# Kernel optimization log

Measured on AMD Instinct MI355X. Metric: run time of the kernel, lower is better.

## Reference

```python
import jax, jax.numpy as jnp
import numpy as np

TMP = 1.0          # concrete temperature (beta)
SAMPLE_BIAS = 0.0  # self.sample_bias

N_NODES = 10000
N_EDGES = 640000
D_EMB = 128
HIDDEN = 64


def setup_inputs() -> dict:
    key = jax.random.key(0)
    k_emb, k_ei, k_w1, k_w2 = jax.random.split(key, 4)
    embed = jax.random.normal(k_emb, (N_NODES, D_EMB), dtype=jnp.float32)
    edge_index = jax.random.randint(k_ei, (2, N_EDGES), 0, N_NODES, dtype=jnp.int64)
    W1 = jax.random.normal(k_w1, (2 * D_EMB, HIDDEN), dtype=jnp.float32) * 0.06
    b1 = jnp.zeros((HIDDEN,), dtype=jnp.float32)
    W2 = jax.random.normal(k_w2, (HIDDEN, 1), dtype=jnp.float32) * 0.12
    b2 = jnp.zeros((1,), dtype=jnp.float32)
    return {"embed": embed, "edge_index": edge_index, "W1": W1, "b1": b1, "W2": W2, "b2": b2}


def _concrete_sample(log_alpha, beta, key):
    # training=True branch: logistic noise through sigmoid gate
    u = jax.random.uniform(key, log_alpha.shape, dtype=log_alpha.dtype)
    u = u * (1.0 - 2.0 * SAMPLE_BIAS) + SAMPLE_BIAS
    noise = jnp.log(u) - jnp.log1p(-u)
    return jax.nn.sigmoid((noise + log_alpha) / beta)


def reference(embed, edge_index, W1, b1, W2, b2):
    N = embed.shape[0]
    col, row = edge_index[0], edge_index[1]
    # edge gather + concat: [E, 2*D]
    f12 = jnp.concatenate([embed[col], embed[row]], axis=-1)
    # tiny 2-layer MLP -> per-edge logit
    h = jax.nn.relu(f12 @ W1 + b1)
    log_alpha = (h @ W2 + b2).reshape(-1)  # [E]
    values = _concrete_sample(log_alpha, TMP, jax.random.key(42))
    # sparse_coo_tensor(...).to_dense() sums duplicate indices
    adj = jnp.zeros((N, N), dtype=embed.dtype).at[col, row].add(1.0)
    mask_dense = jnp.zeros((N, N), dtype=embed.dtype).at[col, row].add(values)
    sym_mask = (mask_dense + mask_dense.T) * 0.5
    masked_adj = adj * sym_mask
    return masked_adj
```

## Files before the change

kernel.cpp:

```cpp
#include <hip/hip_runtime.h>
#include <stdint.h>

#define D_EMB 128
#define HIDDEN 64
#define PACK_SCALE 1024.0f
#define INV_PACK (1.0f/1024.0f)
#define PN 32

__device__ __forceinline__ uint32_t rotl32(uint32_t x, int r) {
    return (x << r) | (x >> (32 - r));
}

__device__ __forceinline__ uint32_t jax_threefry_bits_part(uint32_t e) {
    const uint32_t ks0 = 0u;
    const uint32_t ks1 = 42u;
    const uint32_t ks2 = 0x1BD11BDAu ^ 0u ^ 42u;
    uint32_t x0 = 0u + ks0;
    uint32_t x1 = e + ks1;
#define TF_R(r) { x0 += x1; x1 = rotl32(x1, (r)); x1 ^= x0; }
    TF_R(13) TF_R(15) TF_R(26) TF_R(6)
    x0 += ks1; x1 += ks2 + 1u;
    TF_R(17) TF_R(29) TF_R(16) TF_R(24)
    x0 += ks2; x1 += ks0 + 2u;
    TF_R(13) TF_R(15) TF_R(26) TF_R(6)
    x0 += ks0; x1 += ks1 + 3u;
    TF_R(17) TF_R(29) TF_R(16) TF_R(24)
    x0 += ks1; x1 += ks2 + 4u;
    TF_R(13) TF_R(15) TF_R(26) TF_R(6)
    x0 += ks2; x1 += ks0 + 5u;
#undef TF_R
    return x0 ^ x1;
}

__device__ __forceinline__ float edge_gate_value(
    const float* __restrict__ Pcat, const float* __restrict__ w2s, float b2v,
    int c, int r, int e) {
    const float4* p1 = (const float4*)(Pcat + (size_t)c * (2 * HIDDEN));
    const float4* p2 = (const float4*)(Pcat + (size_t)r * (2 * HIDDEN) + HIDDEN);
    const float4* w4 = (const float4*)w2s;
    float la = b2v;
#pragma unroll
    for (int k = 0; k < HIDDEN / 4; k++) {
        float4 a = p1[k];
        float4 b = p2[k];
        float4 w = w4[k];
        la += fmaxf(a.x + b.x, 0.0f) * w.x + fmaxf(a.y + b.y, 0.0f) * w.y +
              fmaxf(a.z + b.z, 0.0f) * w.z + fmaxf(a.w + b.w, 0.0f) * w.w;
    }
    uint32_t bits = jax_threefry_bits_part((uint32_t)e);
    float u = __uint_as_float((bits >> 9) | 0x3f800000u) - 1.0f;
    return u / (u + (1.0f - u) * __expf(-la));
}

__global__ __launch_bounds__(256) void node_proj_kernel(
    const float* __restrict__ embed, const float* __restrict__ W1,
    const float* __restrict__ b1, float* __restrict__ Pcat, int N) {
    __shared__ float e_lds[PN][D_EMB];
    int n0 = blockIdx.x * PN;
    int t = threadIdx.x;
    {
        const float4* src = (const float4*)embed + (size_t)n0 * (D_EMB / 4);
        float4* dst = (float4*)&e_lds[0][0];
        for (int i = t; i < PN * (D_EMB / 4); i += 256) {
            int node = n0 + (i >> 5);
            float4 v = make_float4(0.f, 0.f, 0.f, 0.f);
            if (node < N) v = src[i];
            dst[i] = v;
        }
    }
    __syncthreads();
    int col = t & 127;
    int nset = t >> 7;
    int half = col >> 6, k = col & 63;
    const float* w = W1 + (size_t)half * D_EMB * HIDDEN + k;
    float bias = (half == 0) ? b1[k] : 0.0f;
    float acc[16];
#pragma unroll
    for (int j = 0; j < 16; j++) acc[j] = bias;
    const int nb = nset * 16;
#pragma unroll 8
    for (int d = 0; d < D_EMB; d++) {
        float wd = w[(size_t)d * HIDDEN];
#pragma unroll
        for (int j = 0; j < 16; j++) acc[j] += e_lds[nb + j][d] * wd;
    }
#pragma unroll
    for (int j = 0; j < 16; j++) {
        int node = n0 + nb + j;
        if (node < N) Pcat[(size_t)node * (2 * HIDDEN) + col] = acc[j];
    }
}

__global__ __launch_bounds__(256) void edge_scatter_kernel(
    const int* __restrict__ ei, const float* __restrict__ Pcat,
    const float* __restrict__ W2, const float* __restrict__ b2,
    float* __restrict__ out, int E, int N) {
    __shared__ float w2s[HIDDEN];
    if (threadIdx.x < HIDDEN) w2s[threadIdx.x] = W2[threadIdx.x];
    __syncthreads();
    int e = blockIdx.x * blockDim.x + threadIdx.x;
    if (e >= E) return;
    int c = ei[e];
    int r = ei[E + e];
    if ((unsigned)c >= (unsigned)N || (unsigned)r >= (unsigned)N) return;
    float v = edge_gate_value(Pcat, w2s, b2[0], c, r, e);
    atomicAdd(out + (size_t)c * N + r, PACK_SCALE + v);
}

__global__ __launch_bounds__(256) void edge_finalize_kernel(
    const int* __restrict__ ei, float* __restrict__ out, int E, int N) {
    int e = blockIdx.x * blockDim.x + threadIdx.x;
    if (e >= E) return;
    int c = ei[e];
    int r = ei[E + e];
    if ((unsigned)c >= (unsigned)N || (unsigned)r >= (unsigned)N) return;

    size_t own = (size_t)c * N + r;
    size_t mir = (size_t)r * N + c;
    float a = out[own];
    if (a < PACK_SCALE) return;
    float b = out[mir];
    if (c != r && b > 0.0f && b < PACK_SCALE) return;

    if (c <= r || b == 0.0f) {
        float cnt_a = truncf(a * INV_PACK);
        float s_a = a - PACK_SCALE * cnt_a;
        float cnt_b = truncf(b * INV_PACK);
        float s_b = b - PACK_SCALE * cnt_b;
        float sum = s_a + s_b;
        out[own] = cnt_a * 0.5f * sum;
        if (c < r && b != 0.0f) out[mir] = cnt_b * 0.5f * sum;
    }
}

extern "C" void kernel_launch(void* const* d_in, const int* in_sizes, int n_in,
                              void* d_out, int out_size, void* d_ws, size_t ws_size,
                              hipStream_t stream) {
    const float* embed = (const float*)d_in[0];
    const int*   ei    = (const int*)d_in[1];
    const float* W1    = (const float*)d_in[2];
    const float* b1    = (const float*)d_in[3];
    const float* W2    = (const float*)d_in[4];
    const float* b2    = (const float*)d_in[5];
    float* out = (float*)d_out;

    const int N = in_sizes[0] / D_EMB;
    const int E = in_sizes[1] / 2;

    float* Pcat = (float*)d_ws;

    hipMemsetAsync(d_out, 0, (size_t)out_size * sizeof(float), stream);

    node_proj_kernel<<<(N + PN - 1) / PN, 256, 0, stream>>>(embed, W1, b1, Pcat, N);

    const int eb = 256;
    const int eg = (E + eb - 1) / eb;
    edge_scatter_kernel<<<eg, eb, 0, stream>>>(ei, Pcat, W2, b2, out, E, N);
    edge_finalize_kernel<<<eg, eb, 0, stream>>>(ei, out, E, N);
}
```

Before: 228.4 us.

## Accumulate edges in hash table and bitmap, then write dense output once

Edge values are accumulated into a global open-addressing hash table keyed by cell index, and a per-cell occupancy bitmap is recorded. A single dense pass then writes every float4 of the output, looking up only occupied cells in the table and combining each with its mirror. This replaces the separate full-output memset plus scattered atomics and finalize pass with one streaming write. The cost is a memset of the table and the 12.5 MB bitmap, plus CAS-based probing; the new path only runs when the workspace is large enough, otherwise it falls back to the old path.

After: 297.4 us. +30.2%, slower.

```diff
diff --git a/kernel.cpp b/kernel.cpp
--- a/kernel.cpp
+++ b/kernel.cpp
@@ -6,6 +6,7 @@
 #define PACK_SCALE 1024.0f
 #define INV_PACK (1.0f/1024.0f)
 #define PN 32
+#define LOG_SZ 21
 
 __device__ __forceinline__ uint32_t rotl32(uint32_t x, int r) {
     return (x << r) | (x >> (32 - r));
@@ -91,6 +92,75 @@
     }
 }
 
+__global__ __launch_bounds__(256) void scatter_hash_kernel(
+    const int* __restrict__ ei, const float* __restrict__ Pcat,
+    const float* __restrict__ W2, const float* __restrict__ b2,
+    uint32_t* __restrict__ tab, uint32_t* __restrict__ bitmap, int E, int N) {
+    __shared__ float w2s[HIDDEN];
+    if (threadIdx.x < HIDDEN) w2s[threadIdx.x] = W2[threadIdx.x];
+    __syncthreads();
+    int e = blockIdx.x * blockDim.x + threadIdx.x;
+    if (e >= E) return;
+    int c = ei[e];
+    int r = ei[E + e];
+    if ((unsigned)c >= (unsigned)N || (unsigned)r >= (unsigned)N) return;
+
+    float v = edge_gate_value(Pcat, w2s, b2[0], c, r, e);
+
+    uint32_t key = (uint32_t)c * (uint32_t)N + (uint32_t)r;
+    atomicOr(&bitmap[key >> 5], 1u << (key & 31));
+
+    const uint32_t mask = (1u << LOG_SZ) - 1u;
+    uint32_t h = (key * 2654435761u) >> (32 - LOG_SZ);
+    for (;;) {
+        uint32_t prev = atomicCAS(&tab[2 * h], 0u, key + 1u);
+        if (prev == 0u || prev == key + 1u) break;
+        h = (h + 1u) & mask;
+    }
+    atomicAdd((float*)&tab[2 * h + 1], PACK_SCALE + v);
+}
+
+__device__ __forceinline__ float hash_lookup(
+    const uint32_t* __restrict__ tab, uint32_t key) {
+    const uint32_t mask = (1u << LOG_SZ) - 1u;
+    uint32_t h = (key * 2654435761u) >> (32 - LOG_SZ);
+    for (;;) {
+        uint2 ent = ((const uint2*)tab)[h];
+        if (ent.x == key + 1u) return __uint_as_float(ent.y);
+        if (ent.x == 0u) return 0.0f;
+        h = (h + 1u) & mask;
+    }
+}
+
+__global__ __launch_bounds__(256) void dense_write_kernel(
+    const uint32_t* __restrict__ tab, const uint32_t* __restrict__ bitmap,
+    float4* __restrict__ out4, size_t n4, int N) {
+    size_t q = (size_t)blockIdx.x * 256 + threadIdx.x;
+    if (q >= n4) return;
+    uint32_t nib = (bitmap[q >> 3] >> ((q & 7) * 4)) & 0xFu;
+    float4 res = make_float4(0.f, 0.f, 0.f, 0.f);
+    if (nib) {
+        float* rp = (float*)&res;
+#pragma unroll
+        for (int j = 0; j < 4; j++) {
+            if (nib & (1u << j)) {
+                uint32_t cell = (uint32_t)(q * 4 + j);
+                uint32_t c = cell / (uint32_t)N;
+                uint32_t r = cell - c * (uint32_t)N;
+                float a = hash_lookup(tab, cell);
+                float m = hash_lookup(tab, r * (uint32_t)N + c);
+                float cnt_a = truncf(a * INV_PACK);
+                float s_a = a - PACK_SCALE * cnt_a;
+                float cnt_m = truncf(m * INV_PACK);
+                float s_m = m - PACK_SCALE * cnt_m;
+                rp[j] = cnt_a * 0.5f * (s_a + s_m);
+            }
+        }
+    }
+    out4[q] = res;
+}
+
+
 __global__ __launch_bounds__(256) void edge_scatter_kernel(
     const int* __restrict__ ei, const float* __restrict__ Pcat,
     const float* __restrict__ W2, const float* __restrict__ b2,
@@ -114,14 +184,12 @@
     int c = ei[e];
     int r = ei[E + e];
     if ((unsigned)c >= (unsigned)N || (unsigned)r >= (unsigned)N) return;
-
     size_t own = (size_t)c * N + r;
     size_t mir = (size_t)r * N + c;
     float a = out[own];
     if (a < PACK_SCALE) return;
     float b = out[mir];
     if (c != r && b > 0.0f && b < PACK_SCALE) return;
-
     if (c <= r || b == 0.0f) {
         float cnt_a = truncf(a * INV_PACK);
         float s_a = a - PACK_SCALE * cnt_a;
@@ -148,13 +216,27 @@
     const int E = in_sizes[1] / 2;
 
     float* Pcat = (float*)d_ws;
-
-    hipMemsetAsync(d_out, 0, (size_t)out_size * sizeof(float), stream);
-
-    node_proj_kernel<<<(N + PN - 1) / PN, 256, 0, stream>>>(embed, W1, b1, Pcat, N);
+    size_t pcat_bytes = ((size_t)N * 2 * HIDDEN * sizeof(float) + 255) & ~(size_t)255;
+    size_t tab_bytes = (size_t)8 << LOG_SZ;
+    size_t bitmap_bytes = (((size_t)N * N + 31) / 32) * 4;
+    size_t need = pcat_bytes + tab_bytes + bitmap_bytes;
 
     const int eb = 256;
     const int eg = (E + eb - 1) / eb;
-    edge_scatter_kernel<<<eg, eb, 0, stream>>>(ei, Pcat, W2, b2, out, E, N);
-    edge_finalize_kernel<<<eg, eb, 0, stream>>>(ei, out, E, N);
-}
+
+    node_proj_kernel<<<(N + PN - 1) / PN, 256, 0, stream>>>(embed, W1, b1, Pcat, N);
+
+    if (ws_size >= need) {
+        uint32_t* tab = (uint32_t*)((char*)d_ws + pcat_bytes);
+        uint32_t* bitmap = (uint32_t*)((char*)d_ws + pcat_bytes + tab_bytes);
+        hipMemsetAsync(tab, 0, tab_bytes + bitmap_bytes, stream);
+        scatter_hash_kernel<<<eg, eb, 0, stream>>>(ei, Pcat, W2, b2, tab, bitmap, E, N);
+        size_t n4 = (size_t)out_size / 4;
+        uint32_t wblocks = (uint32_t)((n4 + 255) / 256);
+        dense_write_kernel<<<wblocks, 256, 0, stream>>>(tab, bitmap, (float4*)out, n4, N);
+    } else {
+        hipMemsetAsync(d_out, 0, (size_t)out_size * sizeof(float), stream);
+        edge_scatter_kernel<<<eg, eb, 0, stream>>>(ei, Pcat, W2, b2, out, E, N);
+        edge_finalize_kernel<<<eg, eb, 0, stream>>>(ei, out, E, N);
+    }
+}
```
